# Kernel optimization log

Measured on AMD Instinct MI355X. Metric: run time of the kernel, lower is better.

Reference implementation:

```python
import jax, jax.numpy as jnp
import numpy as np

B, T, C = 8, 2048, 1024


def setup_inputs() -> dict:
    key = jax.random.key(0)
    k1, k2, k3, k4 = jax.random.split(key, 4)
    x = jax.random.normal(k1, (B, T, C), dtype=jnp.float32)
    # torch Linear(2C, C) weight is [C, 2C]; we store transposed [2C, C] for xh @ W
    scale_in = 1.0 / np.sqrt(2 * C)
    scale_pr = 1.0 / np.sqrt(C)
    W_f = jax.random.normal(k2, (2 * C, C), dtype=jnp.float32) * scale_in
    W_g = jax.random.normal(k3, (2 * C, C), dtype=jnp.float32) * scale_in
    W_proj = jax.random.normal(k4, (C, C), dtype=jnp.float32) * scale_pr
    return {"x": x, "W_f": W_f, "W_g": W_g, "W_proj": W_proj}


def reference(x, W_f, W_g, W_proj):
    # x: [B, T, C]. Sequential CfC recurrence over T via lax.scan.
    Bv, Tv, Cv = x.shape

    def step(h, x_t):
        # h, x_t: [B, C]
        xh = jnp.concatenate([x_t, h], axis=-1)          # [B, 2C]
        f = jax.nn.sigmoid(xh @ W_f)                      # [B, C]
        g = jnp.tanh(xh @ W_g)                            # [B, C]
        h_new = f * h + (1.0 - f) * g
        return h_new, h_new

    h0 = jnp.zeros((Bv, Cv), dtype=x.dtype)
    _, ys = jax.lax.scan(step, h0, jnp.swapaxes(x, 0, 1))  # ys: [T, B, C]
    y = jnp.swapaxes(ys, 0, 1)                              # [B, T, C]
    return y @ W_proj
```

## Files before the change

### kernel.cpp

```cpp
#include <hip/hip_runtime.h>
#include <hip/hip_bf16.h>
#include <stdint.h>

typedef unsigned short u16;
typedef __attribute__((ext_vector_type(8))) short bh8;
typedef __attribute__((ext_vector_type(4))) float f32x4;

static constexpr int Bv = 8, Tv = 2048, Cv = 1024;
#define SENT_BITS 0x7F800000u

__device__ inline u16 f2bf(float f) {
    unsigned u;
    __builtin_memcpy(&u, &f, 4);
    u = (u + 0x7fffu + ((u >> 16) & 1u)) >> 16;
    return (u16)u;
}
__device__ inline float bf2f(u16 v) {
    unsigned u = ((unsigned)v) << 16;
    float f;
    __builtin_memcpy(&f, &u, 4);
    return f;
}

__global__ void cvt_x(const float* __restrict__ x, u16* __restrict__ xb, int n4) {
    int i = blockIdx.x * blockDim.x + threadIdx.x;
    if (i < n4) {
        float4 v = ((const float4*)x)[i];
        ushort4 o;
        o.x = f2bf(v.x); o.y = f2bf(v.y); o.z = f2bf(v.z); o.w = f2bf(v.w);
        ((ushort4*)xb)[i] = o;
    }
}

__global__ void transpose_cvt(const float* __restrict__ W, u16* __restrict__ WT) {
    __shared__ float tile[32][33];
    int kb = blockIdx.x * 32, nb = blockIdx.y * 32;
    int tx = threadIdx.x, ty = threadIdx.y;
#pragma unroll
    for (int r = 0; r < 32; r += 8)
        tile[ty + r][tx] = W[(size_t)(kb + ty + r) * 1024 + nb + tx];
    __syncthreads();
#pragma unroll
    for (int r = 0; r < 32; r += 8)
        WT[(size_t)(nb + ty + r) * 1024 + kb + tx] = f2bf(tile[tx][ty + r]);
}

template <bool OUT_BF16>
__global__ __launch_bounds__(256, 2) void gemm_bt(const u16* __restrict__ A,
                                                  const u16* __restrict__ BT,
                                                  void* __restrict__ Cout,
                                                  int M, int N, int K) {
    __shared__ uint4 As[2][1024];
    __shared__ uint4 Bs[2][1024];
    const int tid = threadIdx.x;
    const int lane = tid & 63;
    const int w = tid >> 6, wm = w >> 1, wn = w & 1;
    const int nTN = N >> 7;
    const int nwg = gridDim.x;
    const int q = nwg >> 3;
    const int bid = blockIdx.x;
    const int swz = (bid & 7) * q + (bid >> 3);
    const int tm = swz / nTN, tn = swz % nTN;
    const size_t row0 = (size_t)tm * 128;
    const size_t col0 = (size_t)tn * 128;
    const int KT = K >> 6;

    uint4 ra[4], rb[4];

    auto issue_loads = [&](int kt) {
#pragma unroll
        for (int p = 0; p < 4; ++p) {
            int gi = p * 256 + tid;
            int r = gi >> 3, sl = gi & 7;
            ra[p] = *(const uint4*)(A + (row0 + r) * K + (size_t)kt * 64 + sl * 8);
            rb[p] = *(const uint4*)(BT + (col0 + r) * K + (size_t)kt * 64 + sl * 8);
        }
    };
    auto write_lds = [&](int bi) {
#pragma unroll
        for (int p = 0; p < 4; ++p) {
            int gi = p * 256 + tid;
            int r = gi >> 3, sl = gi & 7;
            int ph = sl ^ (r & 7);
            As[bi][r * 8 + ph] = ra[p];
            Bs[bi][r * 8 + ph] = rb[p];
        }
    };

    f32x4 acc[4][4];
#pragma unroll
    for (int m = 0; m < 4; ++m)
#pragma unroll
        for (int n = 0; n < 4; ++n)
            acc[m][n] = f32x4{0.f, 0.f, 0.f, 0.f};

    issue_loads(0);
    write_lds(0);
    int cur = 0;
    for (int kt = 0; kt < KT; ++kt) {
        if (kt + 1 < KT) issue_loads(kt + 1);
        __syncthreads();
#pragma unroll
        for (int s = 0; s < 2; ++s) {
            bh8 af[4], bfv[4];
#pragma unroll
            for (int m = 0; m < 4; ++m) {
                int ar = wm * 64 + m * 16 + (lane & 15);
                int sl = (s * 4 + (lane >> 4)) ^ (ar & 7);
                af[m] = __builtin_bit_cast(bh8, As[cur][ar * 8 + sl]);
            }
#pragma unroll
            for (int n = 0; n < 4; ++n) {
                int br = wn * 64 + n * 16 + (lane & 15);
                int sl = (s * 4 + (lane >> 4)) ^ (br & 7);
                bfv[n] = __builtin_bit_cast(bh8, Bs[cur][br * 8 + sl]);
            }
#pragma unroll
            for (int m = 0; m < 4; ++m)
#pragma unroll
                for (int n = 0; n < 4; ++n)
                    acc[m][n] = __builtin_amdgcn_mfma_f32_16x16x32_bf16(af[m], bfv[n], acc[m][n], 0, 0, 0);
        }
        if (kt + 1 < KT) write_lds(cur ^ 1);
        cur ^= 1;
    }
#pragma unroll
    for (int m = 0; m < 4; ++m) {
#pragma unroll
        for (int n = 0; n < 4; ++n) {
#pragma unroll
            for (int r = 0; r < 4; ++r) {
                size_t row = row0 + wm * 64 + m * 16 + (lane >> 4) * 4 + r;
                size_t col = col0 + wn * 64 + n * 16 + (lane & 15);
                float v = acc[m][n][r];
                if (OUT_BF16)
                    ((u16*)Cout)[row * N + col] = f2bf(v);
                else
                    ((float*)Cout)[row * N + col] = v;
            }
        }
    }
}

__global__ void init_hbuf(unsigned* hbuf) {
    int i = blockIdx.x * 1024 + threadIdx.x;
    hbuf[i] = (i < 8192) ? 0u : SENT_BITS;
}

__global__ __launch_bounds__(1024, 4) void cfc_scan(const float* __restrict__ Wf,
                                                    const float* __restrict__ Wg,
                                                    const u16* __restrict__ Pf,
                                                    const u16* __restrict__ Pg,
                                                    u16* __restrict__ H,
                                                    float* hbuf) {
    const int bidx = blockIdx.x;
    const int b = bidx & 7, g = bidx >> 3;
    const int tid = threadIdx.x;
    const int w = tid >> 6;
    const int lane = tid & 63;
    const int slot = lane >> 4;
    const int sub = lane & 15;
    const int col = g * 32 + 2 * w + (slot >> 1);
    const bool isG = (slot & 1) != 0;

    float wreg[64];
    {
        const float* Wsel = isG ? Wg : Wf;
#pragma unroll
        for (int j = 0; j < 64; ++j) {
            int k = (j >> 2) * 64 + sub * 4 + (j & 3);
            wreg[j] = Wsel[(size_t)(1024 + k) * 1024 + col];
        }
    }
    const u16* Psel = isG ? Pg : Pf;
    const size_t prow = (size_t)b * Tv * Cv + col;

    __shared__ __align__(16) float hs[1024];

    float* hb = hbuf + (size_t)b * 1024;
    int bc = 0, bn = 1, bx = 2;

    for (int t = 0; t < Tv; ++t) {
        float p = 0.f;
        if (sub == 0) p = bf2f(Psel[prow + (size_t)t * Cv]);
        __syncthreads();
        {
            const unsigned* src = (const unsigned*)(hb + (size_t)bc * 8192) + tid;
            unsigned v;
            do {
                v = __hip_atomic_load(src, __ATOMIC_RELAXED, __HIP_MEMORY_SCOPE_AGENT);
            } while (v == SENT_BITS);
            hs[tid] = __builtin_bit_cast(float, v);
        }
        __syncthreads();
        if ((lane & 31) == 0)
            __hip_atomic_store((unsigned*)(hb + (size_t)bx * 8192 + col), SENT_BITS,
                               __ATOMIC_RELAXED, __HIP_MEMORY_SCOPE_AGENT);
        float acc = 0.f;
#pragma unroll
        for (int s5 = 0; s5 < 16; ++s5) {
            float4 hv = *(const float4*)&hs[s5 * 64 + sub * 4];
            acc = fmaf(hv.x, wreg[s5 * 4 + 0], acc);
            acc = fmaf(hv.y, wreg[s5 * 4 + 1], acc);
            acc = fmaf(hv.z, wreg[s5 * 4 + 2], acc);
            acc = fmaf(hv.w, wreg[s5 * 4 + 3], acc);
        }
        acc += __shfl_xor(acc, 8);
        acc += __shfl_xor(acc, 4);
        acc += __shfl_xor(acc, 2);
        acc += __shfl_xor(acc, 1);
        float u_ = acc + p;
        float act;
        if (isG) {
            float au = fabsf(u_);
            float e = __expf(-2.f * au);
            float tv = (1.f - e) / (1.f + e);
            act = (u_ < 0.f) ? -tv : tv;
        } else {
            act = 1.f / (1.f + __expf(-u_));
        }
        float other = __shfl_xor(act, 16);
        if ((lane & 31) == 0) {
            float f = act, gv = other;
            float h_old = hs[col];
            float hnew = fmaf(f, h_old - gv, gv);
            asm volatile("s_waitcnt vmcnt(0)" ::: "memory");
            __hip_atomic_store((unsigned*)(hb + (size_t)bn * 8192 + col),
                               __builtin_bit_cast(unsigned, hnew),
                               __ATOMIC_RELAXED, __HIP_MEMORY_SCOPE_AGENT);
            H[prow + (size_t)t * Cv] = f2bf(hnew);
        }
        int tmp = bc; bc = bn; bn = bx; bx = tmp;
    }
}

extern "C" void kernel_launch(void* const* d_in, const int* in_sizes, int n_in,
                              void* d_out, int out_size, void* d_ws, size_t ws_size,
                              hipStream_t stream) {
    const float* x  = (const float*)d_in[0];
    const float* Wf = (const float*)d_in[1];
    const float* Wg = (const float*)d_in[2];
    const float* Wp = (const float*)d_in[3];
    float* out = (float*)d_out;
    char* ws = (char*)d_ws;

    u16*   xb    = (u16*)(ws + 0);
    u16*   Pf    = (u16*)(ws + 33554432);
    u16*   Pg    = (u16*)(ws + 67108864);
    u16*   Hb    = (u16*)(ws + 100663296);
    u16*   WfT   = (u16*)(ws + 134217728);
    u16*   WgT   = (u16*)(ws + 136314880);
    u16*   WpT   = (u16*)(ws + 138412032);
    float* hbuf  = (float*)(ws + 0);

    cvt_x<<<16384, 256, 0, stream>>>(x, xb, (Bv * Tv * Cv) / 4);

    dim3 tg(32, 32), tb(32, 8);
    transpose_cvt<<<tg, tb, 0, stream>>>(Wf, WfT);
    transpose_cvt<<<tg, tb, 0, stream>>>(Wg, WgT);
    transpose_cvt<<<tg, tb, 0, stream>>>(Wp, WpT);

    gemm_bt<true><<<1024, 256, 0, stream>>>(xb, WfT, (void*)Pf, Bv * Tv, Cv, Cv);
    gemm_bt<true><<<1024, 256, 0, stream>>>(xb, WgT, (void*)Pg, Bv * Tv, Cv, Cv);

    init_hbuf<<<24, 1024, 0, stream>>>((unsigned*)hbuf);

    {
        const float* a0 = Wf;
        const float* a1 = Wg;
        const u16* a2 = Pf;
        const u16* a3 = Pg;
        u16* a4 = Hb;
        float* a5 = hbuf;
        void* args[] = {(void*)&a0, (void*)&a1, (void*)&a2, (void*)&a3,
                        (void*)&a4, (void*)&a5};
        hipLaunchCooperativeKernel((const void*)cfc_scan, dim3(256), dim3(1024), args, 0, stream);
    }

    gemm_bt<false><<<1024, 256, 0, stream>>>(Hb, WpT, (void*)out, Bv * Tv, Cv, Cv);
}
```

Before: 4.366 ms.

## Publish hidden state to per-timestep write-once buffer and double-buffer LDS to drop a barrier

Adds a per-timestep write-once array of hidden states, kept in the output buffer and pre-filled with sentinels. Consumers poll it with sc0 loads and only occasionally fall back to the triple-rotated buffer, which removes the race between clearing a slot and reusing it. The shared h buffer and the P values are double-buffered and prefetched by one wave, so the first __syncthreads per step can go. Other changes are four independent FMA accumulators and a single sigmoid-based formula covering both tanh and sigmoid. The costs are an extra 64MB initialisation kernel and a dependence on non-coherent load semantics for correctness.

```diff
diff --git a/kernel.cpp b/kernel.cpp
--- a/kernel.cpp
+++ b/kernel.cpp
@@ -147,12 +147,18 @@
     hbuf[i] = (i < 8192) ? 0u : SENT_BITS;
 }
 
+__global__ void init_hA(uint4* hA4) {
+    int i = blockIdx.x * 1024 + threadIdx.x;
+    unsigned v = (i < 2048) ? 0u : SENT_BITS;
+    hA4[i] = uint4{v, v, v, v};
+}
+
 __global__ __launch_bounds__(1024, 4) void cfc_scan(const float* __restrict__ Wf,
                                                     const float* __restrict__ Wg,
                                                     const u16* __restrict__ Pf,
                                                     const u16* __restrict__ Pg,
                                                     u16* __restrict__ H,
-                                                    float* hbuf) {
+                                                    float* hbuf, float* hA) {
     const int bidx = blockIdx.x;
     const int b = bidx & 7, g = bidx >> 3;
     const int tid = threadIdx.x;
@@ -162,73 +168,88 @@
     const int sub = lane & 15;
     const int col = g * 32 + 2 * w + (slot >> 1);
     const bool isG = (slot & 1) != 0;
-
-    float wreg[64];
-    {
-        const float* Wsel = isG ? Wg : Wf;
-#pragma unroll
-        for (int j = 0; j < 64; ++j) {
-            int k = (j >> 2) * 64 + sub * 4 + (j & 3);
-            wreg[j] = Wsel[(size_t)(1024 + k) * 1024 + col];
-        }
-    }
-    const u16* Psel = isG ? Pg : Pf;
-    const size_t prow = (size_t)b * Tv * Cv + col;
-
-    __shared__ __align__(16) float hs[1024];
-
+    const float cm = isG ? -2.f : -1.f;
+    const float sm = isG ? 2.f : 1.f;
+    const float ofs = isG ? -1.f : 0.f;
+
+    const float* wb = (isG ? Wg : Wf) + (size_t)(1024 + sub * 4) * 1024 + col;
+#define LDW(i) const float4 w##i = {wb[(size_t)((i)*64 + 0) * 1024], wb[(size_t)((i)*64 + 1) * 1024], \
+                                    wb[(size_t)((i)*64 + 2) * 1024], wb[(size_t)((i)*64 + 3) * 1024]};
+    LDW(0) LDW(1) LDW(2) LDW(3) LDW(4) LDW(5) LDW(6) LDW(7)
+    LDW(8) LDW(9) LDW(10) LDW(11) LDW(12) LDW(13) LDW(14) LDW(15)
+#undef LDW
+
+    __shared__ __align__(16) float hs[2][1024];
+    __shared__ u16 ps[2][64];
+
+    const u16* pptr = nullptr;
+    u16 pcur = 0;
+    if (w == 0) {
+        const u16* pa = (lane < 32) ? Pf : Pg;
+        pptr = pa + (size_t)b * Tv * Cv + g * 32 + (lane & 31);
+        pcur = pptr[0];
+    }
+
+    const size_t hrow = (size_t)b * Tv * Cv + col;
     float* hb = hbuf + (size_t)b * 1024;
+    const unsigned* abase = (const unsigned*)hA + b * 1024 + tid;
+    unsigned* apub = (unsigned*)hA + b * 1024 + col;
     int bc = 0, bn = 1, bx = 2;
 
     for (int t = 0; t < Tv; ++t) {
-        float p = 0.f;
-        if (sub == 0) p = bf2f(Psel[prow + (size_t)t * Cv]);
-        __syncthreads();
-        {
-            const unsigned* src = (const unsigned*)(hb + (size_t)bc * 8192) + tid;
-            unsigned v;
-            do {
-                v = __hip_atomic_load(src, __ATOMIC_RELAXED, __HIP_MEMORY_SCOPE_AGENT);
-            } while (v == SENT_BITS);
-            hs[tid] = __builtin_bit_cast(float, v);
+        const unsigned* asrc = abase + (size_t)t * 8192;
+        const unsigned* bsrc = (const unsigned*)(hb + (size_t)bc * 8192) + tid;
+        unsigned v;
+        int spins = 0;
+        while (true) {
+            if ((spins & 3) != 3) {
+                asm volatile("global_load_dword %0, %1, off sc0\n\ts_waitcnt vmcnt(0)"
+                             : "=v"(v) : "v"(asrc) : "memory");
+            } else {
+                v = __hip_atomic_load(bsrc, __ATOMIC_RELAXED, __HIP_MEMORY_SCOPE_AGENT);
+            }
+            if (v != SENT_BITS) break;
+            ++spins;
+        }
+        const int tb = t & 1;
+        hs[tb][tid] = __builtin_bit_cast(float, v);
+        if (w == 0) {
+            ps[tb][lane] = pcur;
+            if (t + 1 < Tv) pcur = pptr[(size_t)(t + 1) * Cv];
         }
         __syncthreads();
         if ((lane & 31) == 0)
             __hip_atomic_store((unsigned*)(hb + (size_t)bx * 8192 + col), SENT_BITS,
                                __ATOMIC_RELAXED, __HIP_MEMORY_SCOPE_AGENT);
-        float acc = 0.f;
-#pragma unroll
-        for (int s5 = 0; s5 < 16; ++s5) {
-            float4 hv = *(const float4*)&hs[s5 * 64 + sub * 4];
-            acc = fmaf(hv.x, wreg[s5 * 4 + 0], acc);
-            acc = fmaf(hv.y, wreg[s5 * 4 + 1], acc);
-            acc = fmaf(hv.z, wreg[s5 * 4 + 2], acc);
-            acc = fmaf(hv.w, wreg[s5 * 4 + 3], acc);
-        }
+        const float* hsrd = hs[tb];
+        float ax = 0.f, ay = 0.f, az = 0.f, aw = 0.f;
+#define MAC(i) { const float4 hv = *(const float4*)&hsrd[(i)*64 + sub * 4]; \
+                 ax = fmaf(hv.x, w##i.x, ax); ay = fmaf(hv.y, w##i.y, ay);  \
+                 az = fmaf(hv.z, w##i.z, az); aw = fmaf(hv.w, w##i.w, aw); }
+        MAC(0) MAC(1) MAC(2) MAC(3) MAC(4) MAC(5) MAC(6) MAC(7)
+        MAC(8) MAC(9) MAC(10) MAC(11) MAC(12) MAC(13) MAC(14) MAC(15)
+#undef MAC
+        float acc = (ax + ay) + (az + aw);
         acc += __shfl_xor(acc, 8);
         acc += __shfl_xor(acc, 4);
         acc += __shfl_xor(acc, 2);
         acc += __shfl_xor(acc, 1);
+        float p = 0.f;
+        if (sub == 0) p = bf2f(ps[tb][((slot & 1) << 5) + 2 * w + (slot >> 1)]);
         float u_ = acc + p;
-        float act;
-        if (isG) {
-            float au = fabsf(u_);
-            float e = __expf(-2.f * au);
-            float tv = (1.f - e) / (1.f + e);
-            act = (u_ < 0.f) ? -tv : tv;
-        } else {
-            act = 1.f / (1.f + __expf(-u_));
-        }
+        float act = fmaf(1.f / (1.f + __expf(cm * u_)), sm, ofs);
         float other = __shfl_xor(act, 16);
         if ((lane & 31) == 0) {
-            float f = act, gv = other;
-            float h_old = hs[col];
-            float hnew = fmaf(f, h_old - gv, gv);
+            float f_ = act, gv = other;
+            float h_old = hsrd[col];
+            float hnew = fmaf(f_, h_old - gv, gv);
+            unsigned hbits = __builtin_bit_cast(unsigned, hnew);
             asm volatile("s_waitcnt vmcnt(0)" ::: "memory");
-            __hip_atomic_store((unsigned*)(hb + (size_t)bn * 8192 + col),
-                               __builtin_bit_cast(unsigned, hnew),
+            if (t + 1 < Tv)
+                *(volatile unsigned*)(apub + (size_t)(t + 1) * 8192) = hbits;
+            __hip_atomic_store((unsigned*)(hb + (size_t)bn * 8192 + col), hbits,
                                __ATOMIC_RELAXED, __HIP_MEMORY_SCOPE_AGENT);
-            H[prow + (size_t)t * Cv] = f2bf(hnew);
+            H[hrow + (size_t)t * Cv] = f2bf(hnew);
         }
         int tmp = bc; bc = bn; bn = bx; bx = tmp;
     }
@@ -252,6 +273,7 @@
     u16*   WgT   = (u16*)(ws + 136314880);
     u16*   WpT   = (u16*)(ws + 138412032);
     float* hbuf  = (float*)(ws + 0);
+    float* hA    = out;
 
     cvt_x<<<16384, 256, 0, stream>>>(x, xb, (Bv * Tv * Cv) / 4);
 
@@ -264,6 +286,7 @@
     gemm_bt<true><<<1024, 256, 0, stream>>>(xb, WgT, (void*)Pg, Bv * Tv, Cv, Cv);
 
     init_hbuf<<<24, 1024, 0, stream>>>((unsigned*)hbuf);
+    init_hA<<<4096, 1024, 0, stream>>>((uint4*)hA);
 
     {
         const float* a0 = Wf;
@@ -272,8 +295,9 @@
         const u16* a3 = Pg;
         u16* a4 = Hb;
         float* a5 = hbuf;
+        float* a6 = hA;
         void* args[] = {(void*)&a0, (void*)&a1, (void*)&a2, (void*)&a3,
-                        (void*)&a4, (void*)&a5};
+                        (void*)&a4, (void*)&a5, (void*)&a6};
         hipLaunchCooperativeKernel((const void*)cfc_scan, dim3(256), dim3(1024), args, 0, stream);
     }
 
```

Result: slower. 8.414 ms (+92.7%).
